# Kernel tuning notes

Measured on AMD Instinct MI355X. Metric: run time of the kernel, lower is better.

The kernel has to match this reference:

```python
import jax, jax.numpy as jnp
import numpy as np

N_LAYERS = 3
NUM_USERS = 100_000
NUM_ITEMS = 100_000
EMB_DIM = 64
NNZ = 2_000_000


def setup_inputs() -> dict:
    key = jax.random.key(0)
    k1, k2, k3, k4, k5 = jax.random.split(key, 5)
    n_nodes = NUM_USERS + 1 + NUM_ITEMS  # 200001
    user_emb = jax.random.normal(k1, (NUM_USERS + 1, EMB_DIM), dtype=jnp.float32) * 0.1
    user_emb = user_emb.at[0].set(0.0)  # padding_idx=0
    item_emb = jax.random.normal(k2, (NUM_ITEMS + 1, EMB_DIM), dtype=jnp.float32) * 0.1
    item_emb = item_emb.at[0].set(0.0)  # padding_idx=0
    adj_rows = jax.random.randint(k3, (NNZ,), 0, n_nodes, dtype=jnp.int32)
    adj_cols = jax.random.randint(k4, (NNZ,), 0, n_nodes, dtype=jnp.int32)
    # symmetric-normalized adjacency values are small positive numbers
    adj_vals = jax.random.uniform(k5, (NNZ,), dtype=jnp.float32) * 0.1
    return {
        "user_emb": user_emb,
        "item_emb": item_emb,
        "adj_rows": adj_rows,
        "adj_cols": adj_cols,
        "adj_vals": adj_vals,
    }


def _spmm(adj_rows, adj_cols, adj_vals, x, n_nodes):
    # y[r] = sum over nnz with row==r of val * x[col]  (COO SpMM)
    msgs = adj_vals[:, None] * x[adj_cols]  # [nnz, d]
    return jax.ops.segment_sum(msgs, adj_rows, num_segments=n_nodes)


def reference(user_emb, item_emb, adj_rows, adj_cols, adj_vals):
    n_users_p1 = user_emb.shape[0]
    all_emb = jnp.concatenate([user_emb, item_emb[1:]], axis=0)  # [N, d]
    n_nodes = all_emb.shape[0]
    acc = all_emb  # running sum for layer-mean pooling
    x = all_emb
    for _ in range(N_LAYERS):
        x = _spmm(adj_rows, adj_cols, adj_vals, x, n_nodes)
        acc = acc + x
    all_out = acc / jnp.asarray(N_LAYERS + 1, all_emb.dtype)
    user_out = all_out[:n_users_p1]
    item_out = jnp.concatenate(
        [jnp.zeros((1, all_out.shape[1]), all_out.dtype), all_out[n_users_p1:]], axis=0
    )
    return user_out, item_out
```

## Files before the change

kernel.cpp:

```cpp
#include <hip/hip_runtime.h>


#define N_NODES 200001
#define NUP1    100001
#define D       64
#define DV      16
#define DV8     8
#define CHUNK   2048
#define NCHUNK  ((N_NODES + CHUNK - 1) / CHUNK)
#define T_TILE  4096
#define EPT     16
#define CAP     24576

__device__ __forceinline__ unsigned short f2bf(float f) {
  unsigned u = __float_as_uint(f);
  unsigned r = (u + 0x7FFFu + ((u >> 16) & 1u)) >> 16;
  return (unsigned short)r;
}
__device__ __forceinline__ float bf2f(unsigned short h) {
  return __uint_as_float(((unsigned)h) << 16);
}
__device__ __forceinline__ float bflo(unsigned u) { return __uint_as_float(u << 16); }
__device__ __forceinline__ float bfhi(unsigned u) { return __uint_as_float(u & 0xFFFF0000u); }

__global__ __launch_bounds__(256) void init_kernel(
    const float4* __restrict__ user_emb,
    const float4* __restrict__ item_emb,
    ushort4* __restrict__ x0,
    int* __restrict__ bucket_cnt) {
  int idx = blockIdx.x * 256 + threadIdx.x;
  if (idx < NCHUNK) bucket_cnt[idx] = 0;
  if (idx >= N_NODES * DV) return;
  int n = idx >> 4;
  int j = idx & 15;
  float4 v = (n < NUP1) ? user_emb[idx]
                        : item_emb[(size_t)(n - 100000) * DV + j];
  x0[idx] = make_ushort4(f2bf(v.x), f2bf(v.y), f2bf(v.z), f2bf(v.w));
}

__global__ __launch_bounds__(256) void pass1_bucket(
    const int*   __restrict__ rows,
    const int*   __restrict__ cols,
    const float* __restrict__ vals,
    int*  __restrict__ bucket_cnt,
    int2* __restrict__ bucket_arr,
    int nnz) {
  __shared__ int lcount[NCHUNK];
  __shared__ int lbase[NCHUNK];
  int t = threadIdx.x;
  for (int i = t; i < NCHUNK; i += 256) lcount[i] = 0;
  __syncthreads();
  long base = (long)blockIdx.x * T_TILE;
  int2 pk[EPT];
  int  meta[EPT];
#pragma unroll
  for (int k = 0; k < EPT; ++k) {
    long e = base + t + (long)k * 256;
    if (e < nnz) {
      int r = rows[e];
      int b = r >> 11;
      int rank = atomicAdd(&lcount[b], 1);
      pk[k] = make_int2(((r & 2047) << 18) | cols[e], __float_as_int(vals[e]));
      meta[k] = (rank << 7) | b;
    } else {
      meta[k] = -1;
    }
  }
  __syncthreads();
  for (int b = t; b < NCHUNK; b += 256) {
    int c = lcount[b];
    lbase[b] = (c > 0) ? (b * CAP + atomicAdd(&bucket_cnt[b], c)) : 0;
  }
  __syncthreads();
#pragma unroll
  for (int k = 0; k < EPT; ++k) {
    if (meta[k] >= 0) {
      int b = meta[k] & 127;
      int rank = meta[k] >> 7;
      bucket_arr[lbase[b] + rank] = pk[k];
    }
  }
}

__global__ void scan_chunks_kernel(const int* __restrict__ cnt,
                                   int* __restrict__ off,
                                   int* __restrict__ row_ptr) {
  if (threadIdx.x == 0 && blockIdx.x == 0) {
    int run = 0;
    for (int i = 0; i < NCHUNK; ++i) { off[i] = run; run += cnt[i]; }
    row_ptr[N_NODES] = run;
  }
}

__global__ __launch_bounds__(256) void build_csr_chunk(
    const int*  __restrict__ bucket_cnt,
    const int2* __restrict__ bucket_arr,
    const int*  __restrict__ chunk_off,
    int*  __restrict__ row_ptr,
    int2* __restrict__ edge_s) {
  __shared__ int lcnt[CHUNK];
  __shared__ int tsum[256];
  int b = blockIdx.x, t = threadIdx.x;
  for (int i = t; i < CHUNK; i += 256) lcnt[i] = 0;
  __syncthreads();
  int ne = bucket_cnt[b];
  const int2* ba = bucket_arr + (size_t)b * CAP;
  for (int i = t; i < ne; i += 256)
    atomicAdd(&lcnt[ba[i].x >> 18], 1);
  __syncthreads();
  int base = t * 8;
  int local[8];
  int s = 0;
#pragma unroll
  for (int k = 0; k < 8; ++k) { local[k] = lcnt[base + k]; s += local[k]; }
  tsum[t] = s;
  __syncthreads();
  for (int off = 1; off < 256; off <<= 1) {
    int v = (t >= off) ? tsum[t - off] : 0;
    __syncthreads();
    tsum[t] += v;
    __syncthreads();
  }
  int run = tsum[t] - s + chunk_off[b];
  int row0 = b * CHUNK;
#pragma unroll
  for (int k = 0; k < 8; ++k) {
    int idx = base + k;
    if (row0 + idx < N_NODES) row_ptr[row0 + idx] = run;
    lcnt[idx] = run;
    run += local[k];
  }
  __syncthreads();
  for (int i = t; i < ne; i += 256) {
    int2 ed = ba[i];
    int p = atomicAdd(&lcnt[ed.x >> 18], 1);
    edge_s[p] = make_int2(ed.x & 0x3FFFF, ed.y);
  }
}

__global__ __launch_bounds__(256) void spmm_bf16_kernel(
    const int*  __restrict__ row_ptr,
    const int2* __restrict__ edge_s,
    const uint4* __restrict__ x,
    uint4*       __restrict__ y) {
  int t = blockIdx.x * 256 + threadIdx.x;
  int r = t >> 3;
  int j = t & 7;
  if (r >= N_NODES) return;
  int s = row_ptr[r];
  int e = row_ptr[r + 1];
  float a0 = 0.f, a1 = 0.f, a2 = 0.f, a3 = 0.f;
  float a4 = 0.f, a5 = 0.f, a6 = 0.f, a7 = 0.f;
  int k = s;
#define ACCUM(ED, XV) {                                   \
    float v = __int_as_float((ED).y);                     \
    a0 += v * bflo((XV).x); a1 += v * bfhi((XV).x);       \
    a2 += v * bflo((XV).y); a3 += v * bfhi((XV).y);       \
    a4 += v * bflo((XV).z); a5 += v * bfhi((XV).z);       \
    a6 += v * bflo((XV).w); a7 += v * bfhi((XV).w); }
  for (; k + 4 <= e; k += 4) {
    int2 e0 = edge_s[k];
    int2 e1 = edge_s[k + 1];
    int2 e2 = edge_s[k + 2];
    int2 e3 = edge_s[k + 3];
    uint4 x0 = x[(size_t)e0.x * DV8 + j];
    uint4 x1 = x[(size_t)e1.x * DV8 + j];
    uint4 x2 = x[(size_t)e2.x * DV8 + j];
    uint4 x3 = x[(size_t)e3.x * DV8 + j];
    ACCUM(e0, x0); ACCUM(e1, x1); ACCUM(e2, x2); ACCUM(e3, x3);
  }
  for (; k < e; ++k) {
    int2 ed = edge_s[k];
    uint4 xv = x[(size_t)ed.x * DV8 + j];
    ACCUM(ed, xv);
  }
#undef ACCUM
  uint4 o;
  o.x = ((unsigned)f2bf(a1) << 16) | f2bf(a0);
  o.y = ((unsigned)f2bf(a3) << 16) | f2bf(a2);
  o.z = ((unsigned)f2bf(a5) << 16) | f2bf(a4);
  o.w = ((unsigned)f2bf(a7) << 16) | f2bf(a6);
  y[t] = o;
}

__global__ __launch_bounds__(256) void final_kernel(
    const float4*  __restrict__ user_emb,
    const float4*  __restrict__ item_emb,
    const ushort4* __restrict__ y1,
    const ushort4* __restrict__ y2,
    const ushort4* __restrict__ y3,
    float4* __restrict__ out) {
  int idx = blockIdx.x * 256 + threadIdx.x;
  if (idx < DV) {
    out[(size_t)NUP1 * DV + idx] = make_float4(0.f, 0.f, 0.f, 0.f);
  }
  if (idx >= N_NODES * DV) return;
  int n = idx >> 4;
  int j = idx & 15;
  float4 v = (n < NUP1) ? user_emb[idx]
                        : item_emb[(size_t)(n - 100000) * DV + j];
  ushort4 a = y1[idx], b = y2[idx], c = y3[idx];
  float4 o;
  o.x = 0.25f * (v.x + bf2f(a.x) + bf2f(b.x) + bf2f(c.x));
  o.y = 0.25f * (v.y + bf2f(a.y) + bf2f(b.y) + bf2f(c.y));
  o.z = 0.25f * (v.z + bf2f(a.z) + bf2f(b.z) + bf2f(c.z));
  o.w = 0.25f * (v.w + bf2f(a.w) + bf2f(b.w) + bf2f(c.w));
  int rm = (n < NUP1) ? n : n + 1;
  out[(size_t)rm * DV + j] = o;
}

static inline char* align16(char* p) {
  return (char*)(((uintptr_t)p + 15) & ~(uintptr_t)15);
}

extern "C" void kernel_launch(void* const* d_in, const int* in_sizes, int n_in,
                              void* d_out, int out_size, void* d_ws, size_t ws_size,
                              hipStream_t stream) {
  const float* user_emb = (const float*)d_in[0];
  const float* item_emb = (const float*)d_in[1];
  const int*   rows     = (const int*)d_in[2];
  const int*   cols     = (const int*)d_in[3];
  const float* vals     = (const float*)d_in[4];
  const int    nnz      = in_sizes[2];

  const size_t xbytes = (size_t)N_NODES * D * sizeof(unsigned short);
  char* p = (char*)d_ws;
  ushort4* x0 = (ushort4*)p;  p += xbytes;
  ushort4* y1 = (ushort4*)p;  p += xbytes;
  ushort4* y2 = (ushort4*)p;  p += xbytes;
  ushort4* y3 = (ushort4*)p;  p += xbytes;
  int2* bucket_arr = (int2*)y2;
  p = align16(p);
  int2* edge_s = (int2*)p;    p += (size_t)nnz * sizeof(int2);
  p = align16(p);
  int* row_ptr = (int*)p;     p += (size_t)(N_NODES + 1) * sizeof(int);
  p = align16(p);
  int* chunk_off = (int*)p;   p += (size_t)NCHUNK * sizeof(int);
  p = align16(p);
  int* bucket_cnt = (int*)p;  p += (size_t)NCHUNK * sizeof(int);

  float* out = (float*)d_out;

  const int row_elems = N_NODES * DV;
  const int node_grid = (row_elems + 255) / 256;
  const int spmm_grid = (N_NODES * DV8 + 255) / 256;
  const int tile_grid = (nnz + T_TILE - 1) / T_TILE;

  init_kernel<<<node_grid, 256, 0, stream>>>(
      (const float4*)user_emb, (const float4*)item_emb, x0, bucket_cnt);
  pass1_bucket<<<tile_grid, 256, 0, stream>>>(
      rows, cols, vals, bucket_cnt, bucket_arr, nnz);
  scan_chunks_kernel<<<1, 64, 0, stream>>>(bucket_cnt, chunk_off, row_ptr);
  build_csr_chunk<<<NCHUNK, 256, 0, stream>>>(
      bucket_cnt, bucket_arr, chunk_off, row_ptr, edge_s);

  spmm_bf16_kernel<<<spmm_grid, 256, 0, stream>>>(
      row_ptr, edge_s, (const uint4*)x0, (uint4*)y1);
  spmm_bf16_kernel<<<spmm_grid, 256, 0, stream>>>(
      row_ptr, edge_s, (const uint4*)y1, (uint4*)y2);
  spmm_bf16_kernel<<<spmm_grid, 256, 0, stream>>>(
      row_ptr, edge_s, (const uint4*)y2, (uint4*)y3);

  final_kernel<<<node_grid, 256, 0, stream>>>(
      (const float4*)user_emb, (const float4*)item_emb, y1, y2, y3,
      (float4*)out);
}
```

Before: 364.7 us.

## Shrink CSR build chunks, parallelize chunk scan, unroll SpMM by eight with clamped loads

Reduces the row-bucket chunk from 2048 to 512 rows, giving four times as many build_csr_chunk blocks so the CSR build spreads across more of the GPU. The single-thread serial scan over chunk counts becomes a 512-thread shared-memory parallel scan. The SpMM inner loop now issues eight edge and gather loads per iteration, clamping indices and zeroing weights past the row end instead of running a scalar remainder loop. The padded loads waste some bandwidth on short rows, and the bucket capacity per chunk shrinks to 6144, which leaves less headroom against skewed rows.

New measurement: 326.0 us. 1.12x faster.

```diff
diff --git a/kernel.cpp b/kernel.cpp
--- a/kernel.cpp
+++ b/kernel.cpp
@@ -6,11 +6,11 @@
 #define D       64
 #define DV      16
 #define DV8     8
-#define CHUNK   2048
+#define CHUNK   512
 #define NCHUNK  ((N_NODES + CHUNK - 1) / CHUNK)
 #define T_TILE  4096
 #define EPT     16
-#define CAP     24576
+#define CAP     6144
 
 __device__ __forceinline__ unsigned short f2bf(float f) {
   unsigned u = __float_as_uint(f);
@@ -58,10 +58,10 @@
     long e = base + t + (long)k * 256;
     if (e < nnz) {
       int r = rows[e];
-      int b = r >> 11;
+      int b = r >> 9;
       int rank = atomicAdd(&lcount[b], 1);
-      pk[k] = make_int2(((r & 2047) << 18) | cols[e], __float_as_int(vals[e]));
-      meta[k] = (rank << 7) | b;
+      pk[k] = make_int2(((r & 511) << 18) | cols[e], __float_as_int(vals[e]));
+      meta[k] = (rank << 9) | b;
     } else {
       meta[k] = -1;
     }
@@ -75,21 +75,29 @@
 #pragma unroll
   for (int k = 0; k < EPT; ++k) {
     if (meta[k] >= 0) {
-      int b = meta[k] & 127;
-      int rank = meta[k] >> 7;
+      int b = meta[k] & 511;
+      int rank = meta[k] >> 9;
       bucket_arr[lbase[b] + rank] = pk[k];
     }
   }
 }
 
-__global__ void scan_chunks_kernel(const int* __restrict__ cnt,
-                                   int* __restrict__ off,
-                                   int* __restrict__ row_ptr) {
-  if (threadIdx.x == 0 && blockIdx.x == 0) {
-    int run = 0;
-    for (int i = 0; i < NCHUNK; ++i) { off[i] = run; run += cnt[i]; }
-    row_ptr[N_NODES] = run;
-  }
+__global__ __launch_bounds__(512) void scan_chunks_kernel(
+    const int* __restrict__ cnt, int* __restrict__ off,
+    int* __restrict__ row_ptr, int nnz) {
+  __shared__ int sh[512];
+  int t = threadIdx.x;
+  int v = (t < NCHUNK) ? cnt[t] : 0;
+  sh[t] = v;
+  __syncthreads();
+  for (int o = 1; o < 512; o <<= 1) {
+    int u = (t >= o) ? sh[t - o] : 0;
+    __syncthreads();
+    sh[t] += u;
+    __syncthreads();
+  }
+  if (t < NCHUNK) off[t] = sh[t] - v;
+  if (t == 0) row_ptr[N_NODES] = nnz;
 }
 
 __global__ __launch_bounds__(256) void build_csr_chunk(
@@ -101,35 +109,31 @@
   __shared__ int lcnt[CHUNK];
   __shared__ int tsum[256];
   int b = blockIdx.x, t = threadIdx.x;
-  for (int i = t; i < CHUNK; i += 256) lcnt[i] = 0;
+  lcnt[t] = 0; lcnt[t + 256] = 0;
   __syncthreads();
   int ne = bucket_cnt[b];
   const int2* ba = bucket_arr + (size_t)b * CAP;
   for (int i = t; i < ne; i += 256)
     atomicAdd(&lcnt[ba[i].x >> 18], 1);
   __syncthreads();
-  int base = t * 8;
-  int local[8];
-  int s = 0;
-#pragma unroll
-  for (int k = 0; k < 8; ++k) { local[k] = lcnt[base + k]; s += local[k]; }
+  int base = t * 2;
+  int l0 = lcnt[base], l1 = lcnt[base + 1];
+  int s = l0 + l1;
   tsum[t] = s;
   __syncthreads();
-  for (int off = 1; off < 256; off <<= 1) {
-    int v = (t >= off) ? tsum[t - off] : 0;
+  for (int o = 1; o < 256; o <<= 1) {
+    int v = (t >= o) ? tsum[t - o] : 0;
     __syncthreads();
     tsum[t] += v;
     __syncthreads();
   }
   int run = tsum[t] - s + chunk_off[b];
   int row0 = b * CHUNK;
-#pragma unroll
-  for (int k = 0; k < 8; ++k) {
-    int idx = base + k;
-    if (row0 + idx < N_NODES) row_ptr[row0 + idx] = run;
-    lcnt[idx] = run;
-    run += local[k];
-  }
+  if (row0 + base < N_NODES) row_ptr[row0 + base] = run;
+  lcnt[base] = run;
+  run += l0;
+  if (row0 + base + 1 < N_NODES) row_ptr[row0 + base + 1] = run;
+  lcnt[base + 1] = run;
   __syncthreads();
   for (int i = t; i < ne; i += 256) {
     int2 ed = ba[i];
@@ -151,28 +155,39 @@
   int e = row_ptr[r + 1];
   float a0 = 0.f, a1 = 0.f, a2 = 0.f, a3 = 0.f;
   float a4 = 0.f, a5 = 0.f, a6 = 0.f, a7 = 0.f;
-  int k = s;
-#define ACCUM(ED, XV) {                                   \
-    float v = __int_as_float((ED).y);                     \
-    a0 += v * bflo((XV).x); a1 += v * bfhi((XV).x);       \
-    a2 += v * bflo((XV).y); a3 += v * bfhi((XV).y);       \
-    a4 += v * bflo((XV).z); a5 += v * bfhi((XV).z);       \
-    a6 += v * bflo((XV).w); a7 += v * bfhi((XV).w); }
-  for (; k + 4 <= e; k += 4) {
-    int2 e0 = edge_s[k];
-    int2 e1 = edge_s[k + 1];
-    int2 e2 = edge_s[k + 2];
-    int2 e3 = edge_s[k + 3];
+  int last = e - 1;
+#define ACCUM(V, XV) {                                    \
+    a0 += (V) * bflo((XV).x); a1 += (V) * bfhi((XV).x);   \
+    a2 += (V) * bflo((XV).y); a3 += (V) * bfhi((XV).y);   \
+    a4 += (V) * bflo((XV).z); a5 += (V) * bfhi((XV).z);   \
+    a6 += (V) * bflo((XV).w); a7 += (V) * bfhi((XV).w); }
+  for (int g = s; g < e; g += 8) {
+    int2 e0 = edge_s[min(g + 0, last)];
+    int2 e1 = edge_s[min(g + 1, last)];
+    int2 e2 = edge_s[min(g + 2, last)];
+    int2 e3 = edge_s[min(g + 3, last)];
+    int2 e4 = edge_s[min(g + 4, last)];
+    int2 e5 = edge_s[min(g + 5, last)];
+    int2 e6 = edge_s[min(g + 6, last)];
+    int2 e7 = edge_s[min(g + 7, last)];
     uint4 x0 = x[(size_t)e0.x * DV8 + j];
     uint4 x1 = x[(size_t)e1.x * DV8 + j];
     uint4 x2 = x[(size_t)e2.x * DV8 + j];
     uint4 x3 = x[(size_t)e3.x * DV8 + j];
-    ACCUM(e0, x0); ACCUM(e1, x1); ACCUM(e2, x2); ACCUM(e3, x3);
-  }
-  for (; k < e; ++k) {
-    int2 ed = edge_s[k];
-    uint4 xv = x[(size_t)ed.x * DV8 + j];
-    ACCUM(ed, xv);
+    uint4 x4 = x[(size_t)e4.x * DV8 + j];
+    uint4 x5 = x[(size_t)e5.x * DV8 + j];
+    uint4 x6 = x[(size_t)e6.x * DV8 + j];
+    uint4 x7 = x[(size_t)e7.x * DV8 + j];
+    float v0 = __int_as_float(e0.y);
+    float v1 = (g + 1 < e) ? __int_as_float(e1.y) : 0.f;
+    float v2 = (g + 2 < e) ? __int_as_float(e2.y) : 0.f;
+    float v3 = (g + 3 < e) ? __int_as_float(e3.y) : 0.f;
+    float v4 = (g + 4 < e) ? __int_as_float(e4.y) : 0.f;
+    float v5 = (g + 5 < e) ? __int_as_float(e5.y) : 0.f;
+    float v6 = (g + 6 < e) ? __int_as_float(e6.y) : 0.f;
+    float v7 = (g + 7 < e) ? __int_as_float(e7.y) : 0.f;
+    ACCUM(v0, x0); ACCUM(v1, x1); ACCUM(v2, x2); ACCUM(v3, x3);
+    ACCUM(v4, x4); ACCUM(v5, x5); ACCUM(v6, x6); ACCUM(v7, x7);
   }
 #undef ACCUM
   uint4 o;
@@ -250,7 +265,7 @@
       (const float4*)user_emb, (const float4*)item_emb, x0, bucket_cnt);
   pass1_bucket<<<tile_grid, 256, 0, stream>>>(
       rows, cols, vals, bucket_cnt, bucket_arr, nnz);
-  scan_chunks_kernel<<<1, 64, 0, stream>>>(bucket_cnt, chunk_off, row_ptr);
+  scan_chunks_kernel<<<1, 512, 0, stream>>>(bucket_cnt, chunk_off, row_ptr, nnz);
   build_csr_chunk<<<NCHUNK, 256, 0, stream>>>(
       bucket_cnt, bucket_arr, chunk_off, row_ptr, edge_s);
 
```
